# Kernel tuning notes

Measured on AMD Instinct MI355X. Metric: run time of the kernel, lower is better.

Reference implementation:

```python
import jax, jax.numpy as jnp
import numpy as np


def setup_inputs() -> dict:
    key = jax.random.key(0)
    k1, k2 = jax.random.split(key)
    B, H, W, C = 32, 32, 32, 256
    N_EMBED = 1024
    z = jax.random.normal(k1, (B, H, W, C), dtype=jnp.float32)
    emb_weights = jax.random.normal(k2, (N_EMBED, C), dtype=jnp.float32)
    return {"z": z, "emb_weights": emb_weights}


def reference(z, emb_weights):
    # z: (B,H,W,C) -> flatten to (N, C)
    B = z.shape[0]
    C = z.shape[-1]
    z_flat = z.reshape(-1, C)  # (N, C)
    # Squared euclidean distance via ||z||^2 + ||e||^2 - 2 z.e^T
    distance = (
        jnp.sum(z_flat ** 2, axis=1, keepdims=True)          # (N, 1)
        + jnp.sum(emb_weights ** 2, axis=1)                   # (n_embed,)
        - 2.0 * jnp.dot(z_flat, emb_weights.T)                # (N, n_embed)
    )
    min_encoding_indices = jnp.argmin(distance, axis=1)       # (N,)
    z_q = emb_weights[min_encoding_indices].reshape(z.shape)  # (B,H,W,C)
    min_encoding_indices = min_encoding_indices.reshape(B, -1)
    return z_q, min_encoding_indices
```

## Files before the change

kernel.cpp:

```cpp
#include <hip/hip_runtime.h>

#define C_DIM 256
#define NCODE 1024
#define MARGIN 0.02f

typedef __bf16 bf16x8 __attribute__((ext_vector_type(8)));
typedef float f32x4 __attribute__((ext_vector_type(4)));

#define WS_ENORM 0
#define WS_META  4096
#define WS_RLIST 8192
#define WS_BP    139264
#define WS_PB    1187840
#define WS_PBI   1712128

#define GLOAD_LDS16(g, s)                                                            \
  __builtin_amdgcn_global_load_lds(                                                  \
      (const __attribute__((address_space(1))) unsigned int*)(g),                    \
      (__attribute__((address_space(3))) unsigned int*)(s), 16, 0, 0)

__device__ __forceinline__ void bf16split(float x, unsigned short& h, unsigned short& l) {
    unsigned u  = __float_as_uint(x);
    unsigned rh = (u + 0x7FFFu + ((u >> 16) & 1u)) & 0xFFFF0000u;
    float    lf = x - __uint_as_float(rh);
    unsigned ul = __float_as_uint(lf);
    h = (unsigned short)(rh >> 16);
    l = (unsigned short)((ul + 0x7FFFu + ((ul >> 16) & 1u)) >> 16);
}

__global__ __launch_bounds__(256) void prep_misc_kernel(const float* __restrict__ emb,
                                                        float* __restrict__ enorm,
                                                        unsigned* __restrict__ meta) {
    int gid = blockIdx.x * 256 + threadIdx.x;
    if (gid == 0) meta[0] = 0u;
    int row = gid >> 6, lane = gid & 63;
    float4 v = reinterpret_cast<const float4*>(emb)[(size_t)row * 64 + lane];
    float s = v.x * v.x + v.y * v.y + v.z * v.z + v.w * v.w;
    #pragma unroll
    for (int off = 32; off; off >>= 1) s += __shfl_xor(s, off, 64);
    if (lane == 0) enorm[row] = s;
}

__global__ __launch_bounds__(256) void prep_b_kernel(const float* __restrict__ emb,
                                                     unsigned short* __restrict__ bp) {
    int tid = blockIdx.x * 256 + threadIdx.x;
    int j   = tid >> 5;
    int u   = tid & 31;
    int kc  = u >> 2, lg = u & 3;
    const float* src = emb + (size_t)j * C_DIM + kc * 32 + lg * 8;
    float4 v0 = *reinterpret_cast<const float4*>(src);
    float4 v1 = *reinterpret_cast<const float4*>(src + 4);
    float vs[8] = {v0.x, v0.y, v0.z, v0.w, v1.x, v1.y, v1.z, v1.w};
    unsigned short h[8], l[8];
    #pragma unroll
    for (int k = 0; k < 8; ++k) bf16split(vs[k], h[k], l[k]);
    int chunk = j >> 5, nf = (j >> 4) & 1, lr = j & 15;
    int lane  = lg * 16 + lr;
    size_t base = (size_t)chunk * 16384 + (size_t)(nf * 8 + kc) * 512 + lane * 8;
    uint4 hp, lp;
    hp.x = (unsigned)h[0] | ((unsigned)h[1] << 16);
    hp.y = (unsigned)h[2] | ((unsigned)h[3] << 16);
    hp.z = (unsigned)h[4] | ((unsigned)h[5] << 16);
    hp.w = (unsigned)h[6] | ((unsigned)h[7] << 16);
    lp.x = (unsigned)l[0] | ((unsigned)l[1] << 16);
    lp.y = (unsigned)l[2] | ((unsigned)l[3] << 16);
    lp.z = (unsigned)l[4] | ((unsigned)l[5] << 16);
    lp.w = (unsigned)l[6] | ((unsigned)l[7] << 16);
    *reinterpret_cast<uint4*>(bp + base)             = hp;
    *reinterpret_cast<uint4*>(bp + base + 16 * 512)  = lp;
}

__global__ __launch_bounds__(512, 2) void vq_main_kernel(
    const float* __restrict__ z, const unsigned short* __restrict__ bp,
    const float* __restrict__ enorm, float2* __restrict__ pb,
    unsigned* __restrict__ pbi) {
    __shared__ alignas(16) unsigned short Bds[2][16384];
    __shared__ float en_s[512];
    __shared__ float mv1[128][2], mv2[128][2];
    __shared__ unsigned mi[128][2];

    const int t    = threadIdx.x;
    const int w    = t >> 6;
    const int lane = t & 63;
    const int lr   = lane & 15, lg = lane >> 4;
    const int wm   = w >> 1;
    const int ng   = w & 1;
    const int  nh  = blockIdx.x & 1;
    const long r0  = (long)(blockIdx.x >> 1) * 128;
    const unsigned short* bph = bp + (size_t)nh * 16 * 16384;

    #pragma unroll
    for (int round = 0; round < 4; ++round) {
        int f = round * 8 + w;
        GLOAD_LDS16(bph + (size_t)f * 512 + lane * 8, &Bds[0][f * 512]);
    }
    if (t < 512) en_s[t] = enorm[nh * 512 + t];

    bf16x8 ah[2][8], al[2][8];
    #pragma unroll
    for (int m = 0; m < 2; ++m) {
        const float* zr = z + (r0 + wm * 32 + m * 16 + lr) * C_DIM + lg * 8;
        #pragma unroll
        for (int kc = 0; kc < 8; ++kc) {
            float4 v0 = *reinterpret_cast<const float4*>(zr + kc * 32);
            float4 v1 = *reinterpret_cast<const float4*>(zr + kc * 32 + 4);
            float vs[8] = {v0.x, v0.y, v0.z, v0.w, v1.x, v1.y, v1.z, v1.w};
            unsigned short hv[8], lv[8];
            #pragma unroll
            for (int jj = 0; jj < 8; ++jj) bf16split(vs[jj], hv[jj], lv[jj]);
            unsigned hp[4] = {
                (unsigned)hv[0] | ((unsigned)hv[1] << 16), (unsigned)hv[2] | ((unsigned)hv[3] << 16),
                (unsigned)hv[4] | ((unsigned)hv[5] << 16), (unsigned)hv[6] | ((unsigned)hv[7] << 16)};
            unsigned lp[4] = {
                (unsigned)lv[0] | ((unsigned)lv[1] << 16), (unsigned)lv[2] | ((unsigned)lv[3] << 16),
                (unsigned)lv[4] | ((unsigned)lv[5] << 16), (unsigned)lv[6] | ((unsigned)lv[7] << 16)};
            ah[m][kc] = __builtin_bit_cast(bf16x8, *reinterpret_cast<uint4*>(hp));
            al[m][kc] = __builtin_bit_cast(bf16x8, *reinterpret_cast<uint4*>(lp));
        }
    }

    float b1[2][4], b2[2][4]; unsigned i1[2][4];
    #pragma unroll
    for (int m = 0; m < 2; ++m)
        #pragma unroll
        for (int r = 0; r < 4; ++r) { b1[m][r] = 3.4e38f; b2[m][r] = 3.4e38f; i1[m][r] = 0; }

    for (int c = 0; c < 16; ++c) {
        const int cur = c & 1;
        __syncthreads();
        if (c < 15) {
            const unsigned short* src = bph + (size_t)(c + 1) * 16384;
            #pragma unroll
            for (int round = 0; round < 4; ++round) {
                int f = round * 8 + w;
                GLOAD_LDS16(src + (size_t)f * 512 + lane * 8, &Bds[cur ^ 1][f * 512]);
            }
            asm volatile("s_waitcnt vmcnt(4)" ::: "memory");
        } else {
            asm volatile("s_waitcnt vmcnt(0)" ::: "memory");
        }
        __syncthreads();

        f32x4 hh0 = {0.f,0.f,0.f,0.f}, hh1 = {0.f,0.f,0.f,0.f};
        f32x4 hl0 = {0.f,0.f,0.f,0.f}, hl1 = {0.f,0.f,0.f,0.f};
        f32x4 lh0 = {0.f,0.f,0.f,0.f}, lh1 = {0.f,0.f,0.f,0.f};
        const unsigned short* bb = &Bds[cur][(ng * 8) * 512 + lane * 8];
        #pragma unroll
        for (int kc = 0; kc < 8; ++kc) {
            bf16x8 bh = *reinterpret_cast<const bf16x8*>(bb + kc * 512);
            bf16x8 bl = *reinterpret_cast<const bf16x8*>(bb + (16 + kc) * 512);
            hh0 = __builtin_amdgcn_mfma_f32_16x16x32_bf16(ah[0][kc], bh, hh0, 0, 0, 0);
            hh1 = __builtin_amdgcn_mfma_f32_16x16x32_bf16(ah[1][kc], bh, hh1, 0, 0, 0);
            lh0 = __builtin_amdgcn_mfma_f32_16x16x32_bf16(al[0][kc], bh, lh0, 0, 0, 0);
            lh1 = __builtin_amdgcn_mfma_f32_16x16x32_bf16(al[1][kc], bh, lh1, 0, 0, 0);
            hl0 = __builtin_amdgcn_mfma_f32_16x16x32_bf16(ah[0][kc], bl, hl0, 0, 0, 0);
            hl1 = __builtin_amdgcn_mfma_f32_16x16x32_bf16(ah[1][kc], bl, hl1, 0, 0, 0);
        }

        const float    en   = en_s[c * 32 + ng * 16 + lr];
        const unsigned code = (unsigned)(nh * 512 + c * 32 + ng * 16 + lr);
        #pragma unroll
        for (int r = 0; r < 4; ++r) {
            float d0 = fmaf(-2.f, hh0[r] + hl0[r] + lh0[r], en);
            if (d0 < b1[0][r]) { b2[0][r] = b1[0][r]; b1[0][r] = d0; i1[0][r] = code; }
            else if (d0 < b2[0][r]) { b2[0][r] = d0; }
            float d1 = fmaf(-2.f, hh1[r] + hl1[r] + lh1[r], en);
            if (d1 < b1[1][r]) { b2[1][r] = b1[1][r]; b1[1][r] = d1; i1[1][r] = code; }
            else if (d1 < b2[1][r]) { b2[1][r] = d1; }
        }
    }

    #pragma unroll
    for (int m = 0; m < 2; ++m)
        #pragma unroll
        for (int r = 0; r < 4; ++r) {
            float v1 = b1[m][r], v2 = b2[m][r]; unsigned j1 = i1[m][r];
            #pragma unroll
            for (int off = 8; off; off >>= 1) {
                float    ov1 = __shfl_xor(v1, off, 64);
                float    ov2 = __shfl_xor(v2, off, 64);
                unsigned oj1 = (unsigned)__shfl_xor((int)j1, off, 64);
                if (ov1 < v1 || (ov1 == v1 && oj1 < j1)) {
                    v2 = fminf(v1, ov2); v1 = ov1; j1 = oj1;
                } else {
                    v2 = fminf(v2, ov1);
                }
            }
            if (lr == 0) {
                int rowl = wm * 32 + m * 16 + lg * 4 + r;
                mv1[rowl][ng] = v1; mv2[rowl][ng] = v2; mi[rowl][ng] = j1;
            }
        }
    __syncthreads();
    if (t < 128) {
        float B1 = mv1[t][0], B2 = mv2[t][0]; unsigned I1 = mi[t][0];
        float o1 = mv1[t][1], o2 = mv2[t][1]; unsigned O1 = mi[t][1];
        if (o1 < B1 || (o1 == B1 && O1 < I1)) { B2 = fminf(B1, o2); B1 = o1; I1 = O1; }
        else                                  { B2 = fminf(B2, o1); }
        pb [(r0 + t) * 2 + nh] = make_float2(B1, B2);
        pbi[(r0 + t) * 2 + nh] = I1;
    }
}

__global__ __launch_bounds__(256) void finalize_gather_kernel(
    const float* __restrict__ emb, const float2* __restrict__ pb,
    const unsigned* __restrict__ pbi, float* __restrict__ zq,
    float* __restrict__ idx_out, unsigned* __restrict__ meta,
    unsigned* __restrict__ rlist) {
    const long row = (long)blockIdx.x * 4 + (threadIdx.x >> 6);
    const int lane = threadIdx.x & 63;
    float2   p0 = pb [row * 2 + 0], p1 = pb [row * 2 + 1];
    unsigned j0 = pbi[row * 2 + 0], j1 = pbi[row * 2 + 1];
    float B1, B2; unsigned I1;
    if (p1.x < p0.x) { B1 = p1.x; I1 = j1; B2 = fminf(p0.x, p1.y); }
    else             { B1 = p0.x; I1 = j0; B2 = fminf(p0.y, p1.x); }
    if (lane == 0) {
        idx_out[row] = (float)I1;
        if (B2 - B1 <= MARGIN) rlist[atomicAdd(meta, 1u)] = (unsigned)row;
    }
    float4 v = reinterpret_cast<const float4*>(emb)[(size_t)I1 * 64 + lane];
    reinterpret_cast<float4*>(zq)[row * 64 + lane] = v;
}

__global__ __launch_bounds__(256) void rescue_kernel(
    const float* __restrict__ z, const float* __restrict__ emb,
    const float* __restrict__ enorm, const unsigned* __restrict__ meta,
    const unsigned* __restrict__ rlist, float* __restrict__ zq,
    float* __restrict__ idx_out) {
    __shared__ float zrow[C_DIM];
    __shared__ float rd[256];
    __shared__ unsigned rix[256];
    const unsigned cnt = meta[0];
    for (unsigned li = blockIdx.x; li < cnt; li += gridDim.x) {
        unsigned row = rlist[li];
        __syncthreads();
        if (threadIdx.x < 64) {
            float4 v = reinterpret_cast<const float4*>(z)[(size_t)row * 64 + threadIdx.x];
            reinterpret_cast<float4*>(zrow)[threadIdx.x] = v;
        }
        __syncthreads();
        const int c = threadIdx.x;
        float a0 = 0.f, a1 = 0.f, a2 = 0.f, a3 = 0.f;
        const float4* zp = reinterpret_cast<const float4*>(zrow);
        const float4* e0 = reinterpret_cast<const float4*>(emb + (size_t)(c)       * C_DIM);
        const float4* e1 = reinterpret_cast<const float4*>(emb + (size_t)(c + 256) * C_DIM);
        const float4* e2 = reinterpret_cast<const float4*>(emb + (size_t)(c + 512) * C_DIM);
        const float4* e3 = reinterpret_cast<const float4*>(emb + (size_t)(c + 768) * C_DIM);
        #pragma unroll 8
        for (int k = 0; k < 64; ++k) {
            float4 z4 = zp[k];
            float4 f0 = e0[k], f1 = e1[k], f2 = e2[k], f3 = e3[k];
            a0 = fmaf(z4.x, f0.x, a0); a0 = fmaf(z4.y, f0.y, a0);
            a0 = fmaf(z4.z, f0.z, a0); a0 = fmaf(z4.w, f0.w, a0);
            a1 = fmaf(z4.x, f1.x, a1); a1 = fmaf(z4.y, f1.y, a1);
            a1 = fmaf(z4.z, f1.z, a1); a1 = fmaf(z4.w, f1.w, a1);
            a2 = fmaf(z4.x, f2.x, a2); a2 = fmaf(z4.y, f2.y, a2);
            a2 = fmaf(z4.z, f2.z, a2); a2 = fmaf(z4.w, f2.w, a2);
            a3 = fmaf(z4.x, f3.x, a3); a3 = fmaf(z4.y, f3.y, a3);
            a3 = fmaf(z4.z, f3.z, a3); a3 = fmaf(z4.w, f3.w, a3);
        }
        float d0 = fmaf(-2.f, a0, enorm[c]);
        float d1 = fmaf(-2.f, a1, enorm[c + 256]);
        float d2 = fmaf(-2.f, a2, enorm[c + 512]);
        float d3 = fmaf(-2.f, a3, enorm[c + 768]);
        float bd = d0; unsigned bi = (unsigned)c;
        if (d1 < bd) { bd = d1; bi = (unsigned)(c + 256); }
        if (d2 < bd) { bd = d2; bi = (unsigned)(c + 512); }
        if (d3 < bd) { bd = d3; bi = (unsigned)(c + 768); }
        rd[threadIdx.x] = bd; rix[threadIdx.x] = bi;
        __syncthreads();
        for (int s = 128; s; s >>= 1) {
            if (threadIdx.x < (unsigned)s) {
                float od = rd[threadIdx.x + s]; unsigned oi = rix[threadIdx.x + s];
                if (od < rd[threadIdx.x] ||
                    (od == rd[threadIdx.x] && oi < rix[threadIdx.x])) {
                    rd[threadIdx.x] = od; rix[threadIdx.x] = oi;
                }
            }
            __syncthreads();
        }
        unsigned code = rix[0];
        if (threadIdx.x < 64) {
            float4 v = reinterpret_cast<const float4*>(emb)[(size_t)code * 64 + threadIdx.x];
            reinterpret_cast<float4*>(zq)[(size_t)row * 64 + threadIdx.x] = v;
        }
        if (threadIdx.x == 0) idx_out[row] = (float)code;
    }
}

extern "C" void kernel_launch(void* const* d_in, const int* in_sizes, int n_in,
                              void* d_out, int out_size, void* d_ws, size_t ws_size,
                              hipStream_t stream) {
    const float* z   = (const float*)d_in[0];
    const float* emb = (const float*)d_in[1];
    const int n = in_sizes[0] / C_DIM;

    float* zq      = (float*)d_out;
    float* idx_out = zq + (size_t)n * C_DIM;

    char* ws = (char*)d_ws;
    float*          enorm = (float*)(ws + WS_ENORM);
    unsigned*       meta  = (unsigned*)(ws + WS_META);
    unsigned*       rlist = (unsigned*)(ws + WS_RLIST);
    unsigned short* bp    = (unsigned short*)(ws + WS_BP);
    float2*         pb    = (float2*)(ws + WS_PB);
    unsigned*       pbi   = (unsigned*)(ws + WS_PBI);

    prep_misc_kernel<<<256, 256, 0, stream>>>(emb, enorm, meta);
    prep_b_kernel<<<128, 256, 0, stream>>>(emb, bp);
    vq_main_kernel<<<(n / 128) * 2, 512, 0, stream>>>(z, bp, enorm, pb, pbi);
    finalize_gather_kernel<<<n / 4, 256, 0, stream>>>(emb, pb, pbi, zq, idx_out,
                                                      meta, rlist);
    rescue_kernel<<<256, 256, 0, stream>>>(z, emb, enorm, meta, rlist, zq, idx_out);
}
```

Measured before the change: 149.3 us.

## Stream codebook fragments from global into registers instead of LDS staging

Drops the LDS double buffer and block barriers in the main VQ kernel. Each wave now loads codebook MFMA fragments straight from global memory into a register double buffer and covers all 32 codes per chunk itself, so blocks shrink to 256 threads and the cross-wave LDS reduction goes away. This removes the __syncthreads and LDS traffic, but every wave now re-reads the codebook from L2/global with no sharing and uses more accumulator registers. The rescue kernel grid is also doubled.

```diff
diff --git a/kernel.cpp b/kernel.cpp
--- a/kernel.cpp
+++ b/kernel.cpp
@@ -13,11 +13,6 @@
 #define WS_BP    139264
 #define WS_PB    1187840
 #define WS_PBI   1712128
-
-#define GLOAD_LDS16(g, s)                                                            \
-  __builtin_amdgcn_global_load_lds(                                                  \
-      (const __attribute__((address_space(1))) unsigned int*)(g),                    \
-      (__attribute__((address_space(3))) unsigned int*)(s), 16, 0, 0)
 
 __device__ __forceinline__ void bf16split(float x, unsigned short& h, unsigned short& l) {
     unsigned u  = __float_as_uint(x);
@@ -70,36 +65,23 @@
     *reinterpret_cast<uint4*>(bp + base + 16 * 512)  = lp;
 }
 
-__global__ __launch_bounds__(512, 2) void vq_main_kernel(
+__global__ __launch_bounds__(256, 2) void vq_main_kernel(
     const float* __restrict__ z, const unsigned short* __restrict__ bp,
     const float* __restrict__ enorm, float2* __restrict__ pb,
     unsigned* __restrict__ pbi) {
-    __shared__ alignas(16) unsigned short Bds[2][16384];
-    __shared__ float en_s[512];
-    __shared__ float mv1[128][2], mv2[128][2];
-    __shared__ unsigned mi[128][2];
-
     const int t    = threadIdx.x;
     const int w    = t >> 6;
     const int lane = t & 63;
     const int lr   = lane & 15, lg = lane >> 4;
-    const int wm   = w >> 1;
-    const int ng   = w & 1;
     const int  nh  = blockIdx.x & 1;
-    const long r0  = (long)(blockIdx.x >> 1) * 128;
-    const unsigned short* bph = bp + (size_t)nh * 16 * 16384;
-
-    #pragma unroll
-    for (int round = 0; round < 4; ++round) {
-        int f = round * 8 + w;
-        GLOAD_LDS16(bph + (size_t)f * 512 + lane * 8, &Bds[0][f * 512]);
-    }
-    if (t < 512) en_s[t] = enorm[nh * 512 + t];
+    const long r0  = (long)(blockIdx.x >> 1) * 128 + w * 32;
+    const unsigned short* bph = bp + (size_t)nh * 16 * 16384 + lane * 8;
+    const float* enh = enorm + nh * 512;
 
     bf16x8 ah[2][8], al[2][8];
     #pragma unroll
     for (int m = 0; m < 2; ++m) {
-        const float* zr = z + (r0 + wm * 32 + m * 16 + lr) * C_DIM + lg * 8;
+        const float* zr = z + (r0 + m * 16 + lr) * C_DIM + lg * 8;
         #pragma unroll
         for (int kc = 0; kc < 8; ++kc) {
             float4 v0 = *reinterpret_cast<const float4*>(zr + kc * 32);
@@ -125,50 +107,66 @@
         #pragma unroll
         for (int r = 0; r < 4; ++r) { b1[m][r] = 3.4e38f; b2[m][r] = 3.4e38f; i1[m][r] = 0; }
 
+    bf16x8 rbh[2][2], rbl[2][2];
+
+#define LOADB(buf, cbase, kc)                                                         \
+    rbh[buf][0] = *reinterpret_cast<const bf16x8*>((cbase) + ((kc)       ) * 512);    \
+    rbh[buf][1] = *reinterpret_cast<const bf16x8*>((cbase) + ( 8 + (kc)  ) * 512);    \
+    rbl[buf][0] = *reinterpret_cast<const bf16x8*>((cbase) + (16 + (kc)  ) * 512);    \
+    rbl[buf][1] = *reinterpret_cast<const bf16x8*>((cbase) + (24 + (kc)  ) * 512);
+
+    LOADB(0, bph, 0);
+
     for (int c = 0; c < 16; ++c) {
-        const int cur = c & 1;
-        __syncthreads();
-        if (c < 15) {
-            const unsigned short* src = bph + (size_t)(c + 1) * 16384;
-            #pragma unroll
-            for (int round = 0; round < 4; ++round) {
-                int f = round * 8 + w;
-                GLOAD_LDS16(src + (size_t)f * 512 + lane * 8, &Bds[cur ^ 1][f * 512]);
-            }
-            asm volatile("s_waitcnt vmcnt(4)" ::: "memory");
-        } else {
-            asm volatile("s_waitcnt vmcnt(0)" ::: "memory");
-        }
-        __syncthreads();
-
-        f32x4 hh0 = {0.f,0.f,0.f,0.f}, hh1 = {0.f,0.f,0.f,0.f};
-        f32x4 hl0 = {0.f,0.f,0.f,0.f}, hl1 = {0.f,0.f,0.f,0.f};
-        f32x4 lh0 = {0.f,0.f,0.f,0.f}, lh1 = {0.f,0.f,0.f,0.f};
-        const unsigned short* bb = &Bds[cur][(ng * 8) * 512 + lane * 8];
+        const unsigned short* cbase = bph + (size_t)c * 16384;
+        const unsigned short* nbase = cbase + 16384;
+        const float en0 = enh[c * 32 + lr];
+        const float en1 = enh[c * 32 + 16 + lr];
+
+        f32x4 hh[2][2], hl[2][2], lh[2][2];
+        #pragma unroll
+        for (int m = 0; m < 2; ++m)
+            #pragma unroll
+            for (int nf = 0; nf < 2; ++nf) {
+                hh[m][nf] = (f32x4){0.f, 0.f, 0.f, 0.f};
+                hl[m][nf] = (f32x4){0.f, 0.f, 0.f, 0.f};
+                lh[m][nf] = (f32x4){0.f, 0.f, 0.f, 0.f};
+            }
+
         #pragma unroll
         for (int kc = 0; kc < 8; ++kc) {
-            bf16x8 bh = *reinterpret_cast<const bf16x8*>(bb + kc * 512);
-            bf16x8 bl = *reinterpret_cast<const bf16x8*>(bb + (16 + kc) * 512);
-            hh0 = __builtin_amdgcn_mfma_f32_16x16x32_bf16(ah[0][kc], bh, hh0, 0, 0, 0);
-            hh1 = __builtin_amdgcn_mfma_f32_16x16x32_bf16(ah[1][kc], bh, hh1, 0, 0, 0);
-            lh0 = __builtin_amdgcn_mfma_f32_16x16x32_bf16(al[0][kc], bh, lh0, 0, 0, 0);
-            lh1 = __builtin_amdgcn_mfma_f32_16x16x32_bf16(al[1][kc], bh, lh1, 0, 0, 0);
-            hl0 = __builtin_amdgcn_mfma_f32_16x16x32_bf16(ah[0][kc], bl, hl0, 0, 0, 0);
-            hl1 = __builtin_amdgcn_mfma_f32_16x16x32_bf16(ah[1][kc], bl, hl1, 0, 0, 0);
-        }
-
-        const float    en   = en_s[c * 32 + ng * 16 + lr];
-        const unsigned code = (unsigned)(nh * 512 + c * 32 + ng * 16 + lr);
-        #pragma unroll
-        for (int r = 0; r < 4; ++r) {
-            float d0 = fmaf(-2.f, hh0[r] + hl0[r] + lh0[r], en);
-            if (d0 < b1[0][r]) { b2[0][r] = b1[0][r]; b1[0][r] = d0; i1[0][r] = code; }
-            else if (d0 < b2[0][r]) { b2[0][r] = d0; }
-            float d1 = fmaf(-2.f, hh1[r] + hl1[r] + lh1[r], en);
-            if (d1 < b1[1][r]) { b2[1][r] = b1[1][r]; b1[1][r] = d1; i1[1][r] = code; }
-            else if (d1 < b2[1][r]) { b2[1][r] = d1; }
+            const int cur = kc & 1, nxt = cur ^ 1;
+            if (kc < 7) {
+                LOADB(nxt, cbase, kc + 1);
+            } else if (c < 15) {
+                LOADB(nxt, nbase, 0);
+            }
+            #pragma unroll
+            for (int nf = 0; nf < 2; ++nf) {
+                hh[0][nf] = __builtin_amdgcn_mfma_f32_16x16x32_bf16(ah[0][kc], rbh[cur][nf], hh[0][nf], 0, 0, 0);
+                hh[1][nf] = __builtin_amdgcn_mfma_f32_16x16x32_bf16(ah[1][kc], rbh[cur][nf], hh[1][nf], 0, 0, 0);
+                lh[0][nf] = __builtin_amdgcn_mfma_f32_16x16x32_bf16(al[0][kc], rbh[cur][nf], lh[0][nf], 0, 0, 0);
+                lh[1][nf] = __builtin_amdgcn_mfma_f32_16x16x32_bf16(al[1][kc], rbh[cur][nf], lh[1][nf], 0, 0, 0);
+                hl[0][nf] = __builtin_amdgcn_mfma_f32_16x16x32_bf16(ah[0][kc], rbl[cur][nf], hl[0][nf], 0, 0, 0);
+                hl[1][nf] = __builtin_amdgcn_mfma_f32_16x16x32_bf16(ah[1][kc], rbl[cur][nf], hl[1][nf], 0, 0, 0);
+            }
+        }
+
+        #pragma unroll
+        for (int nf = 0; nf < 2; ++nf) {
+            const float    en   = nf ? en1 : en0;
+            const unsigned code = (unsigned)(nh * 512 + c * 32 + nf * 16 + lr);
+            #pragma unroll
+            for (int m = 0; m < 2; ++m)
+                #pragma unroll
+                for (int r = 0; r < 4; ++r) {
+                    float d = fmaf(-2.f, hh[m][nf][r] + hl[m][nf][r] + lh[m][nf][r], en);
+                    if (d < b1[m][r]) { b2[m][r] = b1[m][r]; b1[m][r] = d; i1[m][r] = code; }
+                    else if (d < b2[m][r]) { b2[m][r] = d; }
+                }
         }
     }
+#undef LOADB
 
     #pragma unroll
     for (int m = 0; m < 2; ++m)
@@ -187,19 +185,11 @@
                 }
             }
             if (lr == 0) {
-                int rowl = wm * 32 + m * 16 + lg * 4 + r;
-                mv1[rowl][ng] = v1; mv2[rowl][ng] = v2; mi[rowl][ng] = j1;
-            }
-        }
-    __syncthreads();
-    if (t < 128) {
-        float B1 = mv1[t][0], B2 = mv2[t][0]; unsigned I1 = mi[t][0];
-        float o1 = mv1[t][1], o2 = mv2[t][1]; unsigned O1 = mi[t][1];
-        if (o1 < B1 || (o1 == B1 && O1 < I1)) { B2 = fminf(B1, o2); B1 = o1; I1 = O1; }
-        else                                  { B2 = fminf(B2, o1); }
-        pb [(r0 + t) * 2 + nh] = make_float2(B1, B2);
-        pbi[(r0 + t) * 2 + nh] = I1;
-    }
+                long row = r0 + m * 16 + lg * 4 + r;
+                pb [row * 2 + nh] = make_float2(v1, v2);
+                pbi[row * 2 + nh] = j1;
+            }
+        }
 }
 
 __global__ __launch_bounds__(256) void finalize_gather_kernel(
@@ -308,8 +298,8 @@
 
     prep_misc_kernel<<<256, 256, 0, stream>>>(emb, enorm, meta);
     prep_b_kernel<<<128, 256, 0, stream>>>(emb, bp);
-    vq_main_kernel<<<(n / 128) * 2, 512, 0, stream>>>(z, bp, enorm, pb, pbi);
+    vq_main_kernel<<<(n / 128) * 2, 256, 0, stream>>>(z, bp, enorm, pb, pbi);
     finalize_gather_kernel<<<n / 4, 256, 0, stream>>>(emb, pb, pbi, zq, idx_out,
                                                       meta, rlist);
-    rescue_kernel<<<256, 256, 0, stream>>>(z, emb, enorm, meta, rlist, zq, idx_out);
-}
+    rescue_kernel<<<512, 256, 0, stream>>>(z, emb, enorm, meta, rlist, zq, idx_out);
+}
```

New measurement: 145.5 us. -2.5%, faster.

## Replace codebook-streaming kernel with 256x256 tiled split-bf16 GEMM and 4-way column split

Applied to the files above, without the earlier changes.

The main kernel previously kept a 128-row block of z in registers and streamed half the codebook through LDS. It is replaced by a 256x256 output-tile GEMM that double-buffers both A and B through LDS, uses barrier-phased MFMA with s_setprio, and folds the hi/lo split terms into a K of 768. z is now pre-split into bf16 hi/lo in a separate kernel that uses the output buffer as scratch. Each row's partial top-2 results are written for four column blocks instead of two, and finalize merges four. The aim is higher MFMA utilisation and more data reuse per LDS byte, paid for by an extra pass over z, tighter dependence on the scratch-buffer layout, and losing the index tie-break in the cross-block merge.

```diff
diff --git a/kernel.cpp b/kernel.cpp
--- a/kernel.cpp
+++ b/kernel.cpp
@@ -12,7 +12,7 @@
 #define WS_RLIST 8192
 #define WS_BP    139264
 #define WS_PB    1187840
-#define WS_PBI   1712128
+#define WS_PBI   2236416
 
 #define GLOAD_LDS16(g, s)                                                            \
   __builtin_amdgcn_global_load_lds(                                                  \
@@ -41,22 +41,17 @@
     if (lane == 0) enorm[row] = s;
 }
 
-__global__ __launch_bounds__(256) void prep_b_kernel(const float* __restrict__ emb,
-                                                     unsigned short* __restrict__ bp) {
-    int tid = blockIdx.x * 256 + threadIdx.x;
-    int j   = tid >> 5;
-    int u   = tid & 31;
-    int kc  = u >> 2, lg = u & 3;
-    const float* src = emb + (size_t)j * C_DIM + kc * 32 + lg * 8;
-    float4 v0 = *reinterpret_cast<const float4*>(src);
-    float4 v1 = *reinterpret_cast<const float4*>(src + 4);
+__global__ __launch_bounds__(256) void prep_split_kernel(const float* __restrict__ src,
+                                                         unsigned short* __restrict__ dst) {
+    int gid = blockIdx.x * 256 + threadIdx.x;
+    int row = gid >> 5, seg = gid & 31;
+    const float* s = src + (size_t)row * 256 + seg * 8;
+    float4 v0 = *reinterpret_cast<const float4*>(s);
+    float4 v1 = *reinterpret_cast<const float4*>(s + 4);
     float vs[8] = {v0.x, v0.y, v0.z, v0.w, v1.x, v1.y, v1.z, v1.w};
     unsigned short h[8], l[8];
     #pragma unroll
-    for (int k = 0; k < 8; ++k) bf16split(vs[k], h[k], l[k]);
-    int chunk = j >> 5, nf = (j >> 4) & 1, lr = j & 15;
-    int lane  = lg * 16 + lr;
-    size_t base = (size_t)chunk * 16384 + (size_t)(nf * 8 + kc) * 512 + lane * 8;
+    for (int j = 0; j < 8; ++j) bf16split(vs[j], h[j], l[j]);
     uint4 hp, lp;
     hp.x = (unsigned)h[0] | ((unsigned)h[1] << 16);
     hp.y = (unsigned)h[2] | ((unsigned)h[3] << 16);
@@ -66,139 +61,173 @@
     lp.y = (unsigned)l[2] | ((unsigned)l[3] << 16);
     lp.z = (unsigned)l[4] | ((unsigned)l[5] << 16);
     lp.w = (unsigned)l[6] | ((unsigned)l[7] << 16);
-    *reinterpret_cast<uint4*>(bp + base)             = hp;
-    *reinterpret_cast<uint4*>(bp + base + 16 * 512)  = lp;
-}
-
-__global__ __launch_bounds__(512, 2) void vq_main_kernel(
-    const float* __restrict__ z, const unsigned short* __restrict__ bp,
+    *reinterpret_cast<uint4*>(dst + (size_t)row * 512 + seg * 8)       = hp;
+    *reinterpret_cast<uint4*>(dst + (size_t)row * 512 + 256 + seg * 8) = lp;
+}
+
+#define ACOL(ks) ((((ks) & 3) << 6) + ((ks) >= 8 ? 256 : 0))
+#define BCOL(ks) ((((ks) & 3) << 6) + (((ks) >= 4 && (ks) < 8) ? 256 : 0))
+
+__global__ __launch_bounds__(512, 2) void vq_gemm8_kernel(
+    const unsigned short* __restrict__ ap, const unsigned short* __restrict__ bp,
     const float* __restrict__ enorm, float2* __restrict__ pb,
     unsigned* __restrict__ pbi) {
-    __shared__ alignas(16) unsigned short Bds[2][16384];
-    __shared__ float en_s[512];
-    __shared__ float mv1[128][2], mv2[128][2];
-    __shared__ unsigned mi[128][2];
-
-    const int t    = threadIdx.x;
-    const int w    = t >> 6;
-    const int lane = t & 63;
-    const int lr   = lane & 15, lg = lane >> 4;
-    const int wm   = w >> 1;
-    const int ng   = w & 1;
-    const int  nh  = blockIdx.x & 1;
-    const long r0  = (long)(blockIdx.x >> 1) * 128;
-    const unsigned short* bph = bp + (size_t)nh * 16 * 16384;
-
-    #pragma unroll
-    for (int round = 0; round < 4; ++round) {
-        int f = round * 8 + w;
-        GLOAD_LDS16(bph + (size_t)f * 512 + lane * 8, &Bds[0][f * 512]);
-    }
-    if (t < 512) en_s[t] = enorm[nh * 512 + t];
-
-    bf16x8 ah[2][8], al[2][8];
-    #pragma unroll
-    for (int m = 0; m < 2; ++m) {
-        const float* zr = z + (r0 + wm * 32 + m * 16 + lr) * C_DIM + lg * 8;
+    __shared__ unsigned short AbU[32768];
+    __shared__ unsigned short BbU[32768];
+    __shared__ float en_s[256];
+
+    const int t = threadIdx.x;
+    const int w = t >> 6, lane = t & 63;
+    const int lr = lane & 15, lg = lane >> 4;
+    const int wm = w >> 2, wn = w & 3;
+    const int bid = blockIdx.x;
+    const long r0 = (long)(bid >> 2) * 256;
+    const int  c0 = (bid & 3) * 256;
+
+    if (t < 256) en_s[t] = enorm[c0 + t];
+
+    const unsigned short* AsrcL = ap + (size_t)(r0 + w * 16 + lr) * 512 + lg * 8;
+    const unsigned short* BsrcL = bp + (size_t)(c0 + w * 16 + lr) * 512 + lg * 8;
+    unsigned short* AstW = AbU + w * 1024;
+    unsigned short* BstW = BbU + w * 1024;
+    const unsigned short* Ard[2] = {AbU + wm * 8192 + lane * 8,
+                                    AbU + 16384 + wm * 8192 + lane * 8};
+    const unsigned short* Brd[2] = {BbU + (wn >> 1) * 8192 + (wn & 1) * 4096 + lane * 8,
+                                    BbU + 16384 + (wn >> 1) * 8192 + (wn & 1) * 4096 + lane * 8};
+
+#define STG_A(bf, h, col) {                                                          \
+    GLOAD_LDS16(AsrcL + (h) * 65536 + (col),      AstW + (bf) * 16384 + (h) * 8192); \
+    GLOAD_LDS16(AsrcL + (h) * 65536 + (col) + 32, AstW + (bf) * 16384 + (h) * 8192 + 512); }
+#define STG_B(bf, h, col) {                                                          \
+    GLOAD_LDS16(BsrcL + (h) * 65536 + (col),      BstW + (bf) * 16384 + (h) * 8192); \
+    GLOAD_LDS16(BsrcL + (h) * 65536 + (col) + 32, BstW + (bf) * 16384 + (h) * 8192 + 512); }
+#define RD_A(AR, BUF, MB) {                                                          \
+    _Pragma("unroll") for (int mf = 0; mf < 4; ++mf)                                 \
+      _Pragma("unroll") for (int kc = 0; kc < 2; ++kc)                               \
+        AR[mf * 2 + kc] = *reinterpret_cast<const bf16x8*>(                          \
+            Ard[BUF] + ((MB) + mf) * 1024 + kc * 512); }
+#define RD_B(BUF, NB) {                                                              \
+    _Pragma("unroll") for (int nf = 0; nf < 2; ++nf)                                 \
+      _Pragma("unroll") for (int kc = 0; kc < 2; ++kc)                               \
+        Breg[nf * 2 + kc] = *reinterpret_cast<const bf16x8*>(                        \
+            Brd[BUF] + ((NB) + nf) * 1024 + kc * 512); }
+#define DO_MFMA(AR, MB, NB) {                                                        \
+    _Pragma("unroll") for (int mf = 0; mf < 4; ++mf)                                 \
+      _Pragma("unroll") for (int nf = 0; nf < 2; ++nf) {                             \
+        acc[(MB) + mf][(NB) + nf] = __builtin_amdgcn_mfma_f32_16x16x32_bf16(         \
+            AR[mf * 2 + 0], Breg[nf * 2 + 0], acc[(MB) + mf][(NB) + nf], 0, 0, 0);   \
+        acc[(MB) + mf][(NB) + nf] = __builtin_amdgcn_mfma_f32_16x16x32_bf16(         \
+            AR[mf * 2 + 1], Breg[nf * 2 + 1], acc[(MB) + mf][(NB) + nf], 0, 0, 0); } }
+#define BAR()  __builtin_amdgcn_s_barrier()
+#define LGKM0() asm volatile("s_waitcnt lgkmcnt(0)" ::: "memory")
+#define PRIO(x) __builtin_amdgcn_s_setprio(x)
+
+    f32x4 acc[8][4];
+    #pragma unroll
+    for (int mf = 0; mf < 8; ++mf)
         #pragma unroll
-        for (int kc = 0; kc < 8; ++kc) {
-            float4 v0 = *reinterpret_cast<const float4*>(zr + kc * 32);
-            float4 v1 = *reinterpret_cast<const float4*>(zr + kc * 32 + 4);
-            float vs[8] = {v0.x, v0.y, v0.z, v0.w, v1.x, v1.y, v1.z, v1.w};
-            unsigned short hv[8], lv[8];
-            #pragma unroll
-            for (int jj = 0; jj < 8; ++jj) bf16split(vs[jj], hv[jj], lv[jj]);
-            unsigned hp[4] = {
-                (unsigned)hv[0] | ((unsigned)hv[1] << 16), (unsigned)hv[2] | ((unsigned)hv[3] << 16),
-                (unsigned)hv[4] | ((unsigned)hv[5] << 16), (unsigned)hv[6] | ((unsigned)hv[7] << 16)};
-            unsigned lp[4] = {
-                (unsigned)lv[0] | ((unsigned)lv[1] << 16), (unsigned)lv[2] | ((unsigned)lv[3] << 16),
-                (unsigned)lv[4] | ((unsigned)lv[5] << 16), (unsigned)lv[6] | ((unsigned)lv[7] << 16)};
-            ah[m][kc] = __builtin_bit_cast(bf16x8, *reinterpret_cast<uint4*>(hp));
-            al[m][kc] = __builtin_bit_cast(bf16x8, *reinterpret_cast<uint4*>(lp));
-        }
-    }
-
-    float b1[2][4], b2[2][4]; unsigned i1[2][4];
-    #pragma unroll
-    for (int m = 0; m < 2; ++m)
-        #pragma unroll
-        for (int r = 0; r < 4; ++r) { b1[m][r] = 3.4e38f; b2[m][r] = 3.4e38f; i1[m][r] = 0; }
-
-    for (int c = 0; c < 16; ++c) {
-        const int cur = c & 1;
-        __syncthreads();
-        if (c < 15) {
-            const unsigned short* src = bph + (size_t)(c + 1) * 16384;
-            #pragma unroll
-            for (int round = 0; round < 4; ++round) {
-                int f = round * 8 + w;
-                GLOAD_LDS16(src + (size_t)f * 512 + lane * 8, &Bds[cur ^ 1][f * 512]);
-            }
-            asm volatile("s_waitcnt vmcnt(4)" ::: "memory");
-        } else {
-            asm volatile("s_waitcnt vmcnt(0)" ::: "memory");
-        }
-        __syncthreads();
-
-        f32x4 hh0 = {0.f,0.f,0.f,0.f}, hh1 = {0.f,0.f,0.f,0.f};
-        f32x4 hl0 = {0.f,0.f,0.f,0.f}, hl1 = {0.f,0.f,0.f,0.f};
-        f32x4 lh0 = {0.f,0.f,0.f,0.f}, lh1 = {0.f,0.f,0.f,0.f};
-        const unsigned short* bb = &Bds[cur][(ng * 8) * 512 + lane * 8];
-        #pragma unroll
-        for (int kc = 0; kc < 8; ++kc) {
-            bf16x8 bh = *reinterpret_cast<const bf16x8*>(bb + kc * 512);
-            bf16x8 bl = *reinterpret_cast<const bf16x8*>(bb + (16 + kc) * 512);
-            hh0 = __builtin_amdgcn_mfma_f32_16x16x32_bf16(ah[0][kc], bh, hh0, 0, 0, 0);
-            hh1 = __builtin_amdgcn_mfma_f32_16x16x32_bf16(ah[1][kc], bh, hh1, 0, 0, 0);
-            lh0 = __builtin_amdgcn_mfma_f32_16x16x32_bf16(al[0][kc], bh, lh0, 0, 0, 0);
-            lh1 = __builtin_amdgcn_mfma_f32_16x16x32_bf16(al[1][kc], bh, lh1, 0, 0, 0);
-            hl0 = __builtin_amdgcn_mfma_f32_16x16x32_bf16(ah[0][kc], bl, hl0, 0, 0, 0);
-            hl1 = __builtin_amdgcn_mfma_f32_16x16x32_bf16(ah[1][kc], bl, hl1, 0, 0, 0);
-        }
-
-        const float    en   = en_s[c * 32 + ng * 16 + lr];
-        const unsigned code = (unsigned)(nh * 512 + c * 32 + ng * 16 + lr);
+        for (int nf = 0; nf < 4; ++nf) acc[mf][nf] = (f32x4){0.f, 0.f, 0.f, 0.f};
+
+    {
+        const int a0 = ACOL(0), b0 = BCOL(0), a1 = ACOL(1);
+        STG_A(0, 0, a0); STG_A(0, 1, a0);
+        STG_B(0, 0, b0); STG_B(0, 1, b0);
+        STG_A(1, 0, a1); STG_A(1, 1, a1);
+        asm volatile("s_waitcnt vmcnt(4)" ::: "memory");
+        BAR();
+    }
+
+    bf16x8 Alo[8], Ahi[8], Breg[4];
+
+    #pragma unroll 1
+    for (int it = 0; it < 6; ++it) {
+        const bool pre = it < 5;
+        const int cBb  = BCOL(2 * it + 1);
+        const int cAa2 = pre ? ACOL(2 * it + 2) : 0;
+        const int cBa2 = pre ? BCOL(2 * it + 2) : 0;
+        const int cAb2 = pre ? ACOL(2 * it + 3) : 0;
+
+        RD_A(Alo, 0, 0); RD_B(0, 0);
+        STG_B(1, 0, cBb);
+        BAR(); LGKM0(); PRIO(1); DO_MFMA(Alo, 0, 0); PRIO(0); BAR();
+
+        RD_A(Ahi, 0, 4);
+        STG_B(1, 1, cBb);
+        BAR(); LGKM0(); PRIO(1); DO_MFMA(Ahi, 4, 0); PRIO(0); BAR();
+
+        RD_B(0, 2);
+        if (pre) STG_A(0, 0, cAa2);
+        BAR(); LGKM0(); PRIO(1); DO_MFMA(Alo, 0, 2); PRIO(0); BAR();
+
+        if (pre) STG_A(0, 1, cAa2);
+        BAR(); PRIO(1); DO_MFMA(Ahi, 4, 2); PRIO(0);
+        if (pre) { asm volatile("s_waitcnt vmcnt(4)" ::: "memory"); }
+        else     { asm volatile("s_waitcnt vmcnt(0)" ::: "memory"); }
+        BAR();
+
+        RD_A(Alo, 1, 0); RD_B(1, 0);
+        if (pre) STG_B(0, 0, cBa2);
+        BAR(); LGKM0(); PRIO(1); DO_MFMA(Alo, 0, 0); PRIO(0); BAR();
+
+        RD_A(Ahi, 1, 4);
+        if (pre) STG_B(0, 1, cBa2);
+        BAR(); LGKM0(); PRIO(1); DO_MFMA(Ahi, 4, 0); PRIO(0); BAR();
+
+        RD_B(1, 2);
+        if (pre) STG_A(1, 0, cAb2);
+        BAR(); LGKM0(); PRIO(1); DO_MFMA(Alo, 0, 2); PRIO(0); BAR();
+
+        if (pre) STG_A(1, 1, cAb2);
+        BAR(); PRIO(1); DO_MFMA(Ahi, 4, 2); PRIO(0);
+        if (pre) { asm volatile("s_waitcnt vmcnt(4)" ::: "memory"); }
+        BAR();
+    }
+
+    __syncthreads();
+    float* mv1 = reinterpret_cast<float*>(AbU);
+    float* mv2 = mv1 + 1024;
+    int*   mi  = reinterpret_cast<int*>(BbU);
+
+    #pragma unroll
+    for (int mf = 0; mf < 8; ++mf) {
         #pragma unroll
         for (int r = 0; r < 4; ++r) {
-            float d0 = fmaf(-2.f, hh0[r] + hl0[r] + lh0[r], en);
-            if (d0 < b1[0][r]) { b2[0][r] = b1[0][r]; b1[0][r] = d0; i1[0][r] = code; }
-            else if (d0 < b2[0][r]) { b2[0][r] = d0; }
-            float d1 = fmaf(-2.f, hh1[r] + hl1[r] + lh1[r], en);
-            if (d1 < b1[1][r]) { b2[1][r] = b1[1][r]; b1[1][r] = d1; i1[1][r] = code; }
-            else if (d1 < b2[1][r]) { b2[1][r] = d1; }
-        }
-    }
-
-    #pragma unroll
-    for (int m = 0; m < 2; ++m)
-        #pragma unroll
-        for (int r = 0; r < 4; ++r) {
-            float v1 = b1[m][r], v2 = b2[m][r]; unsigned j1 = i1[m][r];
+            float b1 = 3.4e38f, b2 = 3.4e38f; int i1 = 0;
+            #pragma unroll
+            for (int nf = 0; nf < 4; ++nf) {
+                int cl = wn * 64 + nf * 16 + lr;
+                float d = fmaf(-2.f, acc[mf][nf][r], en_s[cl]);
+                if (d < b1) { b2 = b1; b1 = d; i1 = c0 + cl; }
+                else if (d < b2) { b2 = d; }
+            }
             #pragma unroll
             for (int off = 8; off; off >>= 1) {
-                float    ov1 = __shfl_xor(v1, off, 64);
-                float    ov2 = __shfl_xor(v2, off, 64);
-                unsigned oj1 = (unsigned)__shfl_xor((int)j1, off, 64);
-                if (ov1 < v1 || (ov1 == v1 && oj1 < j1)) {
-                    v2 = fminf(v1, ov2); v1 = ov1; j1 = oj1;
+                float ob1 = __shfl_xor(b1, off, 64);
+                float ob2 = __shfl_xor(b2, off, 64);
+                int   oi1 = __shfl_xor(i1, off, 64);
+                if (ob1 < b1 || (ob1 == b1 && oi1 < i1)) {
+                    b2 = fminf(b1, ob2); b1 = ob1; i1 = oi1;
                 } else {
-                    v2 = fminf(v2, ov1);
+                    b2 = fminf(b2, ob1);
                 }
             }
             if (lr == 0) {
-                int rowl = wm * 32 + m * 16 + lg * 4 + r;
-                mv1[rowl][ng] = v1; mv2[rowl][ng] = v2; mi[rowl][ng] = j1;
+                int rowl = wm * 128 + mf * 16 + lg * 4 + r;
+                mv1[rowl * 4 + wn] = b1; mv2[rowl * 4 + wn] = b2; mi[rowl * 4 + wn] = i1;
             }
         }
+    }
     __syncthreads();
-    if (t < 128) {
-        float B1 = mv1[t][0], B2 = mv2[t][0]; unsigned I1 = mi[t][0];
-        float o1 = mv1[t][1], o2 = mv2[t][1]; unsigned O1 = mi[t][1];
-        if (o1 < B1 || (o1 == B1 && O1 < I1)) { B2 = fminf(B1, o2); B1 = o1; I1 = O1; }
-        else                                  { B2 = fminf(B2, o1); }
-        pb [(r0 + t) * 2 + nh] = make_float2(B1, B2);
-        pbi[(r0 + t) * 2 + nh] = I1;
+    if (t < 256) {
+        float B1 = 3.4e38f, B2 = 3.4e38f; int I1 = 0;
+        #pragma unroll
+        for (int s = 0; s < 4; ++s) {
+            float v1 = mv1[t * 4 + s], v2 = mv2[t * 4 + s]; int j = mi[t * 4 + s];
+            if (v1 < B1) { B2 = fminf(B1, v2); B1 = v1; I1 = j; }
+            else         { B2 = fminf(B2, v1); }
+        }
+        pb [(r0 + t) * 4 + (bid & 3)] = make_float2(B1, B2);
+        pbi[(r0 + t) * 4 + (bid & 3)] = (unsigned)I1;
     }
 }
 
@@ -209,11 +238,14 @@
     unsigned* __restrict__ rlist) {
     const long row = (long)blockIdx.x * 4 + (threadIdx.x >> 6);
     const int lane = threadIdx.x & 63;
-    float2   p0 = pb [row * 2 + 0], p1 = pb [row * 2 + 1];
-    unsigned j0 = pbi[row * 2 + 0], j1 = pbi[row * 2 + 1];
-    float B1, B2; unsigned I1;
-    if (p1.x < p0.x) { B1 = p1.x; I1 = j1; B2 = fminf(p0.x, p1.y); }
-    else             { B1 = p0.x; I1 = j0; B2 = fminf(p0.y, p1.x); }
+    float B1 = 3.4e38f, B2 = 3.4e38f; unsigned I1 = 0;
+    #pragma unroll
+    for (int s = 0; s < 4; ++s) {
+        float2   p = pb [row * 4 + s];
+        unsigned j = pbi[row * 4 + s];
+        if (p.x < B1) { B2 = fminf(B1, p.y); B1 = p.x; I1 = j; }
+        else          { B2 = fminf(B2, p.x); }
+    }
     if (lane == 0) {
         idx_out[row] = (float)I1;
         if (B2 - B1 <= MARGIN) rlist[atomicAdd(meta, 1u)] = (unsigned)row;
@@ -306,9 +338,12 @@
     float2*         pb    = (float2*)(ws + WS_PB);
     unsigned*       pbi   = (unsigned*)(ws + WS_PBI);
 
+    unsigned short* ap = (unsigned short*)d_out;
+
     prep_misc_kernel<<<256, 256, 0, stream>>>(emb, enorm, meta);
-    prep_b_kernel<<<128, 256, 0, stream>>>(emb, bp);
-    vq_main_kernel<<<(n / 128) * 2, 512, 0, stream>>>(z, bp, enorm, pb, pbi);
+    prep_split_kernel<<<128, 256, 0, stream>>>(emb, bp);
+    prep_split_kernel<<<4096, 256, 0, stream>>>(z, ap);
+    vq_gemm8_kernel<<<512, 512, 0, stream>>>(ap, bp, enorm, pb, pbi);
     finalize_gather_kernel<<<n / 4, 256, 0, stream>>>(emb, pb, pbi, zq, idx_out,
                                                       meta, rlist);
     rescue_kernel<<<256, 256, 0, stream>>>(z, emb, enorm, meta, rlist, zq, idx_out);
```

Measured after the change: 167.7 us. +12.4%, slower.
